# Kernel optimization log

Hardware: AMD Instinct MI355X
Metric: run time of the kernel (lower is better)

## Reference

```python
import jax, jax.numpy as jnp
import numpy as np
import math

D_MODEL, D_K, D_V, N_HEADS = 1024, 64, 64, 16

def setup_inputs() -> dict:
    key = jax.random.key(0)
    ks = jax.random.split(key, 5)
    x = jax.random.normal(ks[0], (4, 2048, D_MODEL), dtype=jnp.float32)
    s = 1.0 / math.sqrt(D_MODEL)
    # per-head projection weights, stacked: [H, D, d_k] (equivalent to H separate nn.Linear(D, d_k, bias=False))
    Wq = jax.random.normal(ks[1], (N_HEADS, D_MODEL, D_K), dtype=jnp.float32) * s
    Wk = jax.random.normal(ks[2], (N_HEADS, D_MODEL, D_K), dtype=jnp.float32) * s
    Wv = jax.random.normal(ks[3], (N_HEADS, D_MODEL, D_V), dtype=jnp.float32) * s
    # output projection: Linear(d_value*n_heads, d_model, bias=False) -> [H*d_v, D]
    Wo = jax.random.normal(ks[4], (N_HEADS * D_V, D_MODEL), dtype=jnp.float32) * (1.0 / math.sqrt(N_HEADS * D_V))
    return {"x": x, "Wq": Wq, "Wk": Wk, "Wv": Wv, "Wo": Wo}

def reference(x, Wq, Wk, Wv, Wo):
    d_k = Wq.shape[-1]
    # batched per-head projections (fuses the per-head Python loop into one einsum)
    Q = jnp.einsum('bsd,hdk->bhsk', x, Wq)
    K = jnp.einsum('bsd,hdk->bhsk', x, Wk)
    V = jnp.einsum('bsd,hdv->bhsv', x, Wv)
    scores = jnp.einsum('bhqk,bhsk->bhqs', Q, K) / jnp.sqrt(jnp.asarray(d_k, x.dtype))
    weights = jax.nn.softmax(scores, axis=-1)
    heads = jnp.einsum('bhqs,bhsv->bhqv', weights, V)
    B, H, S, Dv = heads.shape
    # concat heads along last dim (head-major order, matching torch.cat of per-head outputs)
    concat = jnp.transpose(heads, (0, 2, 1, 3)).reshape(B, S, H * Dv)
    return concat @ Wo
```

## Files before the change

kernel.cpp:

```cpp
#include <hip/hip_runtime.h>


typedef __attribute__((ext_vector_type(8))) short bf16x8;
typedef __attribute__((ext_vector_type(4))) float f32x4;
typedef __attribute__((ext_vector_type(4))) unsigned short ushortx4;
typedef __attribute__((ext_vector_type(2))) unsigned int uint2v;

__device__ __forceinline__ unsigned short f2bf(float x) {
    unsigned int u = __float_as_uint(x);
    u += 0x7FFFu + ((u >> 16) & 1u);
    return (unsigned short)(u >> 16);
}
__device__ __forceinline__ unsigned int pack_bf2(float hi, float lo) {
    return __builtin_amdgcn_perm(__float_as_uint(hi), __float_as_uint(lo), 0x07060302u);
}

__device__ __forceinline__ void gload_lds16(const unsigned short* g, unsigned short* lds) {
    __builtin_amdgcn_global_load_lds(
        (const __attribute__((address_space(1))) unsigned int*)g,
        (__attribute__((address_space(3))) unsigned int*)lds,
        16, 0, 0);
}

__global__ __launch_bounds__(256) void pack_all(
    const float* __restrict__ x,
    const float* __restrict__ Wq,
    const float* __restrict__ Wk,
    const float* __restrict__ Wv,
    const float* __restrict__ Wo,
    unsigned short* __restrict__ XB,
    unsigned short* __restrict__ WQKVT,
    unsigned short* __restrict__ WOT)
{
    const int bid = blockIdx.x;
    const int tid = threadIdx.x;
    if (bid < 4096) {
        bf16x8 v;
        size_t base = ((size_t)bid * 256 + tid) * 8;
        float4 f0 = *(const float4*)&x[base];
        float4 f1 = *(const float4*)&x[base + 4];
        v[0] = f2bf(f0.x); v[1] = f2bf(f0.y); v[2] = f2bf(f0.z); v[3] = f2bf(f0.w);
        v[4] = f2bf(f1.x); v[5] = f2bf(f1.y); v[6] = f2bf(f1.z); v[7] = f2bf(f1.w);
        *(bf16x8*)&XB[base] = v;
        return;
    }

    __shared__ float lds[64 * 129];
    const float* src;
    size_t outbase;
    float scale = 1.0f;
    int instride;
    unsigned short* outp;
    if (bid < 4480) {
        const int widx = bid - 4096;
        const int part = widx >> 7;
        const int rem  = widx & 127;
        const int h    = rem >> 3;
        const int chunk = rem & 7;
        const float* W = (part == 0) ? Wq : ((part == 1) ? Wk : Wv);
        src = W + h * 65536 + chunk * 8192;
        instride = 64;
        outbase = ((size_t)(part * 1024 + h * 64)) * 1024 + chunk * 128;
        if (part == 0) scale = 0.125f * 1.44269504088896f;
        outp = WQKVT;
    } else {
        const int oidx = bid - 4480;
        const int kc = oidx >> 4;
        const int nc = oidx & 15;
        src = Wo + (size_t)kc * 128 * 1024 + nc * 64;
        instride = 1024;
        outbase = (size_t)(nc * 64) * 1024 + kc * 128;
        outp = WOT;
    }

    const int r0 = tid >> 4;
    const int c4 = (tid & 15) * 4;
    #pragma unroll
    for (int cc = 0; cc < 8; ++cc) {
        const int r = cc * 16 + r0;
        float4 f = *(const float4*)&src[(size_t)r * instride + c4];
        lds[(c4 + 0) * 129 + r] = f.x * scale;
        lds[(c4 + 1) * 129 + r] = f.y * scale;
        lds[(c4 + 2) * 129 + r] = f.z * scale;
        lds[(c4 + 3) * 129 + r] = f.w * scale;
    }
    __syncthreads();

    const int c = tid >> 2;
    const int s = tid & 3;
    #pragma unroll
    for (int j = 0; j < 4; ++j) {
        bf16x8 v;
        #pragma unroll
        for (int e = 0; e < 8; ++e)
            v[e] = f2bf(lds[c * 129 + s * 32 + j * 8 + e]);
        *(bf16x8*)&outp[outbase + (size_t)c * 1024 + s * 32 + j * 8] = v;
    }
}

template<int CMODE, int BN>
__global__ __launch_bounds__(256) void gemm_bt(
    const unsigned short* __restrict__ A,
    const unsigned short* __restrict__ Bt,
    void* __restrict__ Cv,
    unsigned short* __restrict__ VT,
    int M, int N, int K, int ldc)
{
    __shared__ __align__(16) unsigned short As[2][128 * 32];
    __shared__ __align__(16) unsigned short Bs[2][BN * 32];

    const int flat = blockIdx.y * gridDim.x + blockIdx.x;
    const int cpx  = (gridDim.x * gridDim.y) >> 3;
    const int swz  = (flat & 7) * cpx + (flat >> 3);
    const int m0 = (swz / gridDim.x) * 128;
    const int n0 = (swz % gridDim.x) * BN;

    const int tid  = threadIdx.x;
    const int w    = tid >> 6, lane = tid & 63;
    const int q4   = lane >> 4, lr  = lane & 15;
    constexpr int MI = (BN == 128) ? 4 : 2;
    const int rowBase = (BN == 128) ? (w >> 1) * 64 : w * 32;
    const int colBase = (BN == 128) ? (w & 1) * 64 : 0;

    const int ch   = tid & 3;
    const int row0 = tid >> 2;
    const int ldsOff = w * 512;

    const unsigned short* aP0 = &A [(size_t)(m0 + row0)      * K + ch * 8];
    const unsigned short* aP1 = &A [(size_t)(m0 + row0 + 64) * K + ch * 8];
    const unsigned short* bP0 = &Bt[(size_t)(n0 + row0)      * K + ch * 8];
    const unsigned short* bP1 = (BN == 128)
        ? &Bt[(size_t)(n0 + row0 + 64) * K + ch * 8] : nullptr;

    auto dma = [&](int buf, int k0) {
        gload_lds16(aP0 + k0, &As[buf][ldsOff]);
        gload_lds16(aP1 + k0, &As[buf][2048 + ldsOff]);
        gload_lds16(bP0 + k0, &Bs[buf][ldsOff]);
        if (BN == 128)
            gload_lds16(bP1 + k0, &Bs[buf][2048 + ldsOff]);
    };

    f32x4 acc[MI][4] = {};
    dma(0, 0);
    int cur = 0;

    for (int k0 = 0; k0 < K; k0 += 32) {
        __syncthreads();
        if (k0 + 32 < K) dma(cur ^ 1, k0 + 32);

        bf16x8 af[MI], bfv[4];
        #pragma unroll
        for (int i = 0; i < MI; ++i)
            af[i] = *(const bf16x8*)&As[cur][(rowBase + i * 16 + lr) * 32 + q4 * 8];
        #pragma unroll
        for (int j = 0; j < 4; ++j)
            bfv[j] = *(const bf16x8*)&Bs[cur][(colBase + j * 16 + lr) * 32 + q4 * 8];
        #pragma unroll
        for (int i = 0; i < MI; ++i)
            #pragma unroll
            for (int j = 0; j < 4; ++j)
                acc[i][j] = __builtin_amdgcn_mfma_f32_16x16x32_bf16(af[i], bfv[j], acc[i][j], 0, 0, 0);
        cur ^= 1;
    }

    #pragma unroll
    for (int i = 0; i < MI; ++i) {
        const int row = m0 + rowBase + i * 16 + q4 * 4;
        #pragma unroll
        for (int j = 0; j < 4; ++j) {
            const int col = n0 + colBase + j * 16 + lr;
            if (CMODE == 0) {
                float* C = (float*)Cv;
                #pragma unroll
                for (int p = 0; p < 4; ++p)
                    C[(size_t)(row + p) * ldc + col] = acc[i][j][p];
            } else {
                if (col < 2048) {
                    unsigned short* C = (unsigned short*)Cv;
                    #pragma unroll
                    for (int p = 0; p < 4; ++p)
                        C[(size_t)(row + p) * 2048 + col] = f2bf(acc[i][j][p]);
                } else {
                    const int c2 = col - 2048;
                    const int hh = c2 >> 6, dd = c2 & 63;
                    const int bb = row >> 11, ss = row & 2047;
                    ushortx4 v;
                    #pragma unroll
                    for (int p = 0; p < 4; ++p) v[p] = f2bf(acc[i][j][p]);
                    *(ushortx4*)&VT[((size_t)(bb * 16 + hh) * 64 + dd) * 2048 + ss] = v;
                }
            }
        }
    }
}

__global__ __launch_bounds__(256, 4) void attn_flash(
    const unsigned short* __restrict__ QK,
    const unsigned short* __restrict__ VT,
    unsigned short* __restrict__ HC)
{
    const int bh  = blockIdx.x;
    const int qb  = blockIdx.y;
    const int b   = bh >> 4, h = bh & 15;
    const int tid = threadIdx.x;
    const int w   = tid >> 6, lane = tid & 63;
    const int q4  = lane >> 4, lr  = lane & 15;

    __shared__ __align__(16) unsigned short Ks [2][64 * 64];
    __shared__ __align__(16) unsigned short Vts[2][64 * 64];

    const int drow   = tid >> 3;
    const int gchunk = (tid & 7) ^ (drow & 7);
    const unsigned short* Kg = QK + (size_t)(b * 2048) * 2048 + 1024 + h * 64;
    const unsigned short* Vg = VT + (size_t)bh * 64 * 2048;
    const unsigned short* kP0 = Kg + (size_t)(drow)      * 2048 + gchunk * 8;
    const unsigned short* kP1 = Kg + (size_t)(drow + 32) * 2048 + gchunk * 8;
    const unsigned short* vP0 = Vg + (size_t)(drow)      * 2048 + gchunk * 8;
    const unsigned short* vP1 = Vg + (size_t)(drow + 32) * 2048 + gchunk * 8;
    const int ldsOff = w * 512;

    auto dma = [&](int buf, int t) {
        gload_lds16(kP0 + (size_t)t * 131072, &Ks [buf][ldsOff]);
        gload_lds16(kP1 + (size_t)t * 131072, &Ks [buf][2048 + ldsOff]);
        gload_lds16(vP0 + t * 64,             &Vts[buf][ldsOff]);
        gload_lds16(vP1 + t * 64,             &Vts[buf][2048 + ldsOff]);
    };

    dma(0, 0);

    const int qrow0 = b * 2048 + qb * 128 + w * 32;
    bf16x8 qf[2][2];
    #pragma unroll
    for (int u = 0; u < 2; ++u)
        #pragma unroll
        for (int c = 0; c < 2; ++c)
            qf[u][c] = *(const bf16x8*)&QK[(size_t)(qrow0 + u * 16 + lr) * 2048
                                           + h * 64 + c * 32 + q4 * 8];

    const int lr7 = lr & 7;

    const short oneb = (short)0x3F80;
    const bf16x8 onesf = { oneb, oneb, oneb, oneb, oneb, oneb, oneb, oneb };

    f32x4 o[2][4] = {};
    f32x4 lsum[2] = {};
    int cur = 0;

    for (int t = 0; t < 32; ++t) {
        __syncthreads();
        if (t + 1 < 32) dma(cur ^ 1, t + 1);

        #pragma unroll
        for (int kc = 0; kc < 2; ++kc) {
            unsigned int pk[2][2][2];
            #pragma unroll
            for (int ml = 0; ml < 2; ++ml) {
                const int mt = kc * 2 + ml;
                f32x4 st[2] = {};
                __builtin_amdgcn_s_setprio(1);
                #pragma unroll
                for (int c = 0; c < 2; ++c) {
                    const int slot = (c * 4 + q4) ^ lr7;
                    bf16x8 kf = *(const bf16x8*)&Ks[cur][(mt * 16 + lr) * 64 + slot * 8];
                    #pragma unroll
                    for (int u = 0; u < 2; ++u)
                        st[u] = __builtin_amdgcn_mfma_f32_16x16x32_bf16(kf, qf[u][c], st[u], 0, 0, 0);
                }
                __builtin_amdgcn_s_setprio(0);
                #pragma unroll
                for (int u = 0; u < 2; ++u) {
                    float e0 = __builtin_amdgcn_exp2f(st[u][0]);
                    float e1 = __builtin_amdgcn_exp2f(st[u][1]);
                    float e2 = __builtin_amdgcn_exp2f(st[u][2]);
                    float e3 = __builtin_amdgcn_exp2f(st[u][3]);
                    pk[u][ml][0] = pack_bf2(e1, e0);
                    pk[u][ml][1] = pack_bf2(e3, e2);
                }
            }

            bf16x8 pb[2];
            #pragma unroll
            for (int u = 0; u < 2; ++u) {
                uint2v a0 = __builtin_amdgcn_permlane32_swap(pk[u][0][0], pk[u][1][0], false, false);
                uint2v b0 = __builtin_amdgcn_permlane16_swap(a0[0], a0[1], false, false);
                uint2v a1 = __builtin_amdgcn_permlane32_swap(pk[u][0][1], pk[u][1][1], false, false);
                uint2v b1 = __builtin_amdgcn_permlane16_swap(a1[0], a1[1], false, false);
                int4 wv;
                wv.x = (int)b0[0];
                wv.y = (int)b1[0];
                wv.z = (int)b0[1];
                wv.w = (int)b1[1];
                pb[u] = *(bf16x8*)&wv;
            }

            __builtin_amdgcn_s_setprio(1);
            #pragma unroll
            for (int u = 0; u < 2; ++u)
                lsum[u] = __builtin_amdgcn_mfma_f32_16x16x32_bf16(onesf, pb[u], lsum[u], 0, 0, 0);
            #pragma unroll
            for (int jd = 0; jd < 4; ++jd) {
                const int slot = (kc * 4 + q4) ^ lr7;
                bf16x8 vf = *(const bf16x8*)&Vts[cur][(jd * 16 + lr) * 64 + slot * 8];
                #pragma unroll
                for (int u = 0; u < 2; ++u)
                    o[u][jd] = __builtin_amdgcn_mfma_f32_16x16x32_bf16(vf, pb[u], o[u][jd], 0, 0, 0);
            }
            __builtin_amdgcn_s_setprio(0);
        }
        cur ^= 1;
    }

    #pragma unroll
    for (int u = 0; u < 2; ++u) {
        const float inv = __builtin_amdgcn_rcpf(lsum[u][0]);
        const size_t rowO = (size_t)(qrow0 + u * 16 + lr);
        #pragma unroll
        for (int jd = 0; jd < 4; ++jd) {
            ushortx4 v;
            #pragma unroll
            for (int p = 0; p < 4; ++p)
                v[p] = f2bf(o[u][jd][p] * inv);
            *(ushortx4*)&HC[rowO * 1024 + h * 64 + jd * 16 + q4 * 4] = v;
        }
    }
}

extern "C" void kernel_launch(void* const* d_in, const int* in_sizes, int n_in,
                              void* d_out, int out_size, void* d_ws, size_t ws_size,
                              hipStream_t stream)
{
    const float* x  = (const float*)d_in[0];
    const float* Wq = (const float*)d_in[1];
    const float* Wk = (const float*)d_in[2];
    const float* Wv = (const float*)d_in[3];
    const float* Wo = (const float*)d_in[4];
    float* out = (float*)d_out;

    char* ws = (char*)d_ws;
    unsigned short* XB    = (unsigned short*)(ws);
    unsigned short* HC    = (unsigned short*)(ws);
    unsigned short* WQKVT = (unsigned short*)(ws + 16777216);
    unsigned short* WOT   = (unsigned short*)(ws + 23068672);
    unsigned short* QK    = (unsigned short*)(ws + 25165824);
    unsigned short* VT    = (unsigned short*)(ws + 58720256);

    pack_all<<<4608, 256, 0, stream>>>(x, Wq, Wk, Wv, Wo, XB, WQKVT, WOT);
    gemm_bt<1, 128><<<dim3(24, 64), 256, 0, stream>>>(XB, WQKVT, QK, VT, 8192, 3072, 1024, 0);
    attn_flash<<<dim3(64, 16), 256, 0, stream>>>(QK, VT, HC);
    gemm_bt<0, 128><<<dim3(8, 64), 256, 0, stream>>>(HC, WOT, out, nullptr, 8192, 1024, 1024, 1024);
}
```

Before: 262.8 us.

## Replace QKV projection GEMM with 256x256-tile 8-wave pipelined kernel

Swaps the generic 128-tile QKV projection GEMM for a dedicated kernel that uses 256x256 output tiles with 512 threads. It loads A/B via direct global-to-LDS copies in quarter stages, interleaved with the MFMA work, and raises wave priority around the MFMAs. A block-index swizzle improves L2 locality. The aim is higher arithmetic intensity per LDS byte and better overlap of loads with compute, at the cost of 128KB LDS per block and fewer blocks (384) for the device.

```diff
diff --git a/kernel.cpp b/kernel.cpp
--- a/kernel.cpp
+++ b/kernel.cpp
@@ -194,6 +194,129 @@
     }
 }
 
+__global__ __launch_bounds__(512, 2) void gemm_qkv8(
+    const unsigned short* __restrict__ A,
+    const unsigned short* __restrict__ Bt,
+    unsigned short* __restrict__ QK,
+    unsigned short* __restrict__ VT)
+{
+    constexpr int K = 1024;
+    __shared__ __align__(16) unsigned short As[32768];
+    __shared__ __align__(16) unsigned short Bs[32768];
+
+    const int flat = blockIdx.y * 12 + blockIdx.x;
+    const int swz  = (flat & 7) * 48 + (flat >> 3);
+    const int m0 = (swz / 12) * 256;
+    const int n0 = (swz % 12) * 256;
+
+    const int tid  = threadIdx.x;
+    const int w    = tid >> 6, lane = tid & 63;
+    const int q4   = lane >> 4, lr  = lane & 15;
+    const int wr   = w >> 2, wc = w & 3;
+
+    const unsigned short* pA = A  + (size_t)(m0 + (tid >> 3)) * K + (tid & 7) * 8;
+    const unsigned short* pB = Bt + (size_t)(n0 + (tid >> 3)) * K + (tid & 7) * 8;
+    const int woff = w * 512;
+
+    auto stage = [&](int h) {
+        if (h >= 64) return;
+        const int t = h >> 2, kind = h & 3, buf = t & 1;
+        if (kind >= 2) {
+            const int i = kind - 2;
+            const unsigned short* s = pA + (size_t)(i * 128) * K + t * 64;
+            unsigned short* d = &As[buf * 16384 + i * 8192 + woff];
+            gload_lds16(s, d);
+            gload_lds16(s + (size_t)64 * K, d + 4096);
+        } else {
+            const unsigned short* s = pB + (size_t)(kind * 128) * K + t * 64;
+            unsigned short* d = &Bs[buf * 16384 + kind * 8192 + woff];
+            gload_lds16(s, d);
+            gload_lds16(s + (size_t)64 * K, d + 4096);
+        }
+    };
+
+    stage(0); stage(1); stage(2); stage(3);
+
+    f32x4 acc[8][4] = {};
+
+    for (int t = 0; t < 16; ++t) {
+        const int buf = t & 1;
+        const unsigned short* Ab = &As[buf * 16384 + wr * 8192];
+        const unsigned short* Bb = &Bs[buf * 16384 + (wc >> 1) * 8192];
+        const int brow = (wc & 1) * 64;
+        bf16x8 bf[4][2];
+
+        stage(4 * t + 4);
+        asm volatile("s_waitcnt vmcnt(2)" ::: "memory");
+        __builtin_amdgcn_s_barrier();
+        #pragma unroll
+        for (int n = 0; n < 4; ++n)
+            #pragma unroll
+            for (int ks = 0; ks < 2; ++ks)
+                bf[n][ks] = *(const bf16x8*)&Bb[(brow + n * 16 + lr) * 64 + ks * 32 + q4 * 8];
+        {
+            bf16x8 af[2][2];
+            #pragma unroll
+            for (int mm = 0; mm < 2; ++mm)
+                #pragma unroll
+                for (int ks = 0; ks < 2; ++ks)
+                    af[mm][ks] = *(const bf16x8*)&Ab[(mm * 16 + lr) * 64 + ks * 32 + q4 * 8];
+            __builtin_amdgcn_s_setprio(1);
+            #pragma unroll
+            for (int mm = 0; mm < 2; ++mm)
+                #pragma unroll
+                for (int n = 0; n < 4; ++n)
+                    #pragma unroll
+                    for (int ks = 0; ks < 2; ++ks)
+                        acc[mm][n] = __builtin_amdgcn_mfma_f32_16x16x32_bf16(af[mm][ks], bf[n][ks], acc[mm][n], 0, 0, 0);
+            __builtin_amdgcn_s_setprio(0);
+        }
+
+        #pragma unroll
+        for (int p = 1; p < 4; ++p) {
+            stage(4 * t + 4 + p);
+            __builtin_amdgcn_s_barrier();
+            bf16x8 af[2][2];
+            #pragma unroll
+            for (int mm = 0; mm < 2; ++mm)
+                #pragma unroll
+                for (int ks = 0; ks < 2; ++ks)
+                    af[mm][ks] = *(const bf16x8*)&Ab[(p * 32 + mm * 16 + lr) * 64 + ks * 32 + q4 * 8];
+            __builtin_amdgcn_s_setprio(1);
+            #pragma unroll
+            for (int mm = 0; mm < 2; ++mm)
+                #pragma unroll
+                for (int n = 0; n < 4; ++n)
+                    #pragma unroll
+                    for (int ks = 0; ks < 2; ++ks)
+                        acc[p * 2 + mm][n] = __builtin_amdgcn_mfma_f32_16x16x32_bf16(af[mm][ks], bf[n][ks], acc[p * 2 + mm][n], 0, 0, 0);
+            __builtin_amdgcn_s_setprio(0);
+        }
+    }
+
+    #pragma unroll
+    for (int m = 0; m < 8; ++m) {
+        const int row = m0 + wr * 128 + m * 16 + q4 * 4;
+        #pragma unroll
+        for (int n = 0; n < 4; ++n) {
+            const int col = n0 + wc * 64 + n * 16 + lr;
+            if (col < 2048) {
+                #pragma unroll
+                for (int p = 0; p < 4; ++p)
+                    QK[(size_t)(row + p) * 2048 + col] = f2bf(acc[m][n][p]);
+            } else {
+                const int c2 = col - 2048;
+                const int hh = c2 >> 6, dd = c2 & 63;
+                const int bb = row >> 11, ss = row & 2047;
+                ushortx4 v;
+                #pragma unroll
+                for (int p = 0; p < 4; ++p) v[p] = f2bf(acc[m][n][p]);
+                *(ushortx4*)&VT[((size_t)(bb * 16 + hh) * 64 + dd) * 2048 + ss] = v;
+            }
+        }
+    }
+}
+
 __global__ __launch_bounds__(256, 4) void attn_flash(
     const unsigned short* __restrict__ QK,
     const unsigned short* __restrict__ VT,
@@ -345,7 +468,7 @@
     unsigned short* VT    = (unsigned short*)(ws + 58720256);
 
     pack_all<<<4608, 256, 0, stream>>>(x, Wq, Wk, Wv, Wo, XB, WQKVT, WOT);
-    gemm_bt<1, 128><<<dim3(24, 64), 256, 0, stream>>>(XB, WQKVT, QK, VT, 8192, 3072, 1024, 0);
+    gemm_qkv8<<<dim3(12, 32), 512, 0, stream>>>(XB, WQKVT, QK, VT);
     attn_flash<<<dim3(64, 16), 256, 0, stream>>>(QK, VT, HC);
     gemm_bt<0, 128><<<dim3(8, 64), 256, 0, stream>>>(HC, WOT, out, nullptr, 8192, 1024, 1024, 1024);
 }
```

Measured after the change: 284.1 us. +8.1%, slower.
